# Kernel optimization log

Hardware: AMD Instinct MI355X
Metric: run time of the kernel (lower is better)

## Reference

```python
import jax, jax.numpy as jnp
import numpy as np

B, N, I = 8, 1024, 64
E, H, D = 2, 2, 128   # edge types, heads per layer, hidden dim
O = 64                # num_outputs
IN1 = E * H * D       # layer-1 filter input dim (concat of layer-0 heads)


def setup_inputs() -> dict:
    key = jax.random.key(0)
    ks = jax.random.split(key, 20)
    s = lambda f: 1.0 / np.sqrt(f)
    inp = {
        "nodes": jax.random.normal(ks[0], (B, N, I), jnp.float32),
        "edges": jax.random.normal(ks[1], (B, N, N, E), jnp.float32) * 0.1,
        "Wemb": jax.random.normal(ks[2], (I, D), jnp.float32) * s(I),
        "bemb": jnp.zeros((D,), jnp.float32),
        # layer 0 params: filter W, att nets a1/a2 (weight + bias), state bias
        "W0":   jax.random.normal(ks[3], (E, H, D, D), jnp.float32) * s(D),
        "A1w0": jax.random.normal(ks[4], (E, H, D), jnp.float32) * s(D),
        "A1b0": jnp.zeros((E, H), jnp.float32),
        "A2w0": jax.random.normal(ks[5], (E, H, D), jnp.float32) * s(D),
        "A2b0": jnp.zeros((E, H), jnp.float32),
        "SB0":  jnp.zeros((E, H, D), jnp.float32),
        # layer 1 params (input dim = E*H*D from concat)
        "W1":   jax.random.normal(ks[6], (E, H, IN1, D), jnp.float32) * s(IN1),
        "A1w1": jax.random.normal(ks[7], (E, H, D), jnp.float32) * s(D),
        "A1b1": jnp.zeros((E, H), jnp.float32),
        "A2w1": jax.random.normal(ks[8], (E, H, D), jnp.float32) * s(D),
        "A2b1": jnp.zeros((E, H), jnp.float32),
        "SB1":  jnp.zeros((E, H, D), jnp.float32),
        "Wout": jax.random.normal(ks[9], (D, O), jnp.float32) * s(D),
        "bout": jnp.zeros((O,), jnp.float32),
    }
    return inp


def _gat_layer(state, edges_ebnn, W, a1w, a1b, a2w, a2b, sb):
    # state: (B,N,Fin); W: (E,H,Fin,D); edges_ebnn: (E,1,B,N,N)
    Wh = jnp.einsum('bni,ehid->ehbnd', state, W)                    # (E,H,B,N,D)
    s1 = jnp.einsum('ehbnd,ehd->ehbn', Wh, a1w) + a1b[:, :, None, None]
    s2 = jnp.einsum('ehbnd,ehd->ehbn', Wh, a2w) + a2b[:, :, None, None]
    att = s1[..., :, None] + s2[..., None, :]                       # a1_i + a2_j
    att = jax.nn.leaky_relu(att, 0.2) + edges_ebnn                  # edge-type bias
    att = jax.nn.softmax(att, axis=-2)                              # torch dim=1 (over i)
    msg = jnp.einsum('ehbij,ehbjd->ehbid', att, Wh)                 # bmm aggregation
    return msg + sb[:, :, None, None, :]                            # (E,H,B,N,D)


def reference(nodes, edges, Wemb, bemb,
              W0, A1w0, A1b0, A2w0, A2b0, SB0,
              W1, A1w1, A1b1, A2w1, A2b1, SB1,
              Wout, bout):
    edges_e = jnp.transpose(edges, (3, 0, 1, 2))[:, None]           # (E,1,B,N,N)
    state = jax.nn.relu(nodes @ Wemb + bemb)                        # SlimFC embedding
    # layer 0: concat heads/edgetypes along feature dim (torch order jj outer, ii inner)
    m0 = _gat_layer(state, edges_e, W0, A1w0, A1b0, A2w0, A2b0, SB0)
    state = jnp.transpose(m0, (2, 3, 0, 1, 4)).reshape(B, N, E * H * D)
    # layer 1 (last): elu then mean over all heads/edgetypes
    m1 = jax.nn.elu(_gat_layer(state, edges_e, W1, A1w1, A1b1, A2w1, A2b1, SB1))
    state = jnp.mean(m1, axis=(0, 1))                               # (B,N,D)
    return state @ Wout + bout                                      # (B,N,O)
```

## Files before the change

### kernel.cpp

```cpp
#include <hip/hip_runtime.h>
#include <hip/hip_bf16.h>
#include <math.h>

#define NB 8
#define NN 1024
#define NI 64
#define EHC 4
#define ND 128
#define NO 64
#define FIN1 512
#define BN 8192

typedef __attribute__((ext_vector_type(8))) short short8;
typedef __attribute__((ext_vector_type(4))) float f32x4;

__device__ __forceinline__ unsigned short f2bf(float f) {
    union { float f; unsigned u; } v; v.f = f;
    unsigned r = v.u + 0x7FFF + ((v.u >> 16) & 1);
    return (unsigned short)(r >> 16);
}
__device__ __forceinline__ float bf2f(unsigned short h) {
    union { unsigned u; float f; } v; v.u = ((unsigned)h) << 16;
    return v.f;
}

__global__ void prepTk(const float* __restrict__ W0, const float* __restrict__ W1,
                       unsigned short* __restrict__ W0T, unsigned short* __restrict__ W1T) {
    int idx = blockIdx.x * 256 + threadIdx.x;
    if (idx < EHC * ND * ND) {
        int eh = idx >> 14, d = (idx >> 7) & 127, k = idx & 127;
        W0T[idx] = f2bf(W0[((size_t)(eh * ND + k)) * ND + d]);
    }
    int idx1 = idx - EHC * ND * ND;
    if (idx1 >= 0 && idx1 < EHC * ND * FIN1) {
        int eh = idx1 >> 16;
        int r = idx1 & 65535;
        int d = r >> 9, k = r & 511;
        W1T[idx1] = f2bf(W1[((size_t)(eh * FIN1 + k)) * ND + d]);
    }
}

__global__ __launch_bounds__(256) void embedk(const float* __restrict__ nodes,
                                              const float* __restrict__ Wemb,
                                              const float* __restrict__ bemb,
                                              unsigned short* __restrict__ state0) {
    int row0 = blockIdx.x * 16;
    int t = threadIdx.x;
    __shared__ float wL[NI * ND];
    __shared__ float nL[16 * NI];
    for (int idx = t; idx < NI * ND; idx += 256) wL[idx] = Wemb[idx];
    for (int idx = t; idx < 16 * NI; idx += 256) nL[idx] = nodes[(size_t)row0 * NI + idx];
    __syncthreads();
    int d = t & 127, rh = t >> 7;
    float b0 = bemb[d];
    float acc[8];
#pragma unroll
    for (int r = 0; r < 8; ++r) acc[r] = b0;
#pragma unroll 8
    for (int k = 0; k < NI; ++k) {
        float w = wL[k * ND + d];
#pragma unroll
        for (int r = 0; r < 8; ++r) acc[r] += nL[(rh * 8 + r) * NI + k] * w;
    }
#pragma unroll
    for (int r = 0; r < 8; ++r)
        state0[(size_t)(row0 + rh * 8 + r) * ND + d] = f2bf(fmaxf(acc[r], 0.f));
}

template <int FIN>
__global__ __launch_bounds__(256) void whgemmk(const unsigned short* __restrict__ state,
                                               const unsigned short* __restrict__ WT,
                                               unsigned short* __restrict__ WhT) {
    int eh = blockIdx.y;
    int row0 = blockIdx.x * 64;
    int t = threadIdx.x;
    int w = t >> 6, lane = t & 63;
    int m = lane & 15, quad = lane >> 4;

    f32x4 acc[4][2];
#pragma unroll
    for (int mt = 0; mt < 4; ++mt)
#pragma unroll
        for (int nt = 0; nt < 2; ++nt) acc[mt][nt] = (f32x4){0.f, 0.f, 0.f, 0.f};

    const unsigned short* Ab = state + (size_t)(row0 + m) * FIN + quad * 8;
    const unsigned short* Bb = WT + ((size_t)eh * ND + w * 32 + m) * FIN + quad * 8;
#pragma unroll
    for (int k0 = 0; k0 < FIN; k0 += 32) {
        short8 a[4], b[2];
#pragma unroll
        for (int mt = 0; mt < 4; ++mt)
            a[mt] = *(const short8*)(Ab + (size_t)mt * 16 * FIN + k0);
#pragma unroll
        for (int nt = 0; nt < 2; ++nt)
            b[nt] = *(const short8*)(Bb + (size_t)nt * 16 * FIN + k0);
#pragma unroll
        for (int mt = 0; mt < 4; ++mt)
#pragma unroll
            for (int nt = 0; nt < 2; ++nt)
                acc[mt][nt] =
                    __builtin_amdgcn_mfma_f32_16x16x32_bf16(a[mt], b[nt], acc[mt][nt], 0, 0, 0);
    }
    int b_ = row0 >> 10, i0b = row0 & 1023;
#pragma unroll
    for (int mt = 0; mt < 4; ++mt)
#pragma unroll
        for (int nt = 0; nt < 2; ++nt) {
            int d = w * 32 + nt * 16 + m;
            int i = i0b + mt * 16 + quad * 4;
            union { unsigned short us[4]; unsigned long long u64; } pk;
#pragma unroll
            for (int r = 0; r < 4; ++r) pk.us[r] = f2bf(acc[mt][nt][r]);
            *(unsigned long long*)(WhT + (((size_t)eh * NB + b_) * ND + d) * NN + i) = pk.u64;
        }
}

__global__ __launch_bounds__(256) void s1s2k(const unsigned short* __restrict__ WhT,
                                             const float* __restrict__ a1w,
                                             const float* __restrict__ a1b,
                                             const float* __restrict__ a2w,
                                             const float* __restrict__ a2b,
                                             float* __restrict__ s1, float* __restrict__ s2) {
    int bx = blockIdx.x;
    int ehb = bx >> 4;
    int eh = ehb >> 3;
    int it = bx & 15;
    int i0 = it * 64;
    int t = threadIdx.x;
    int il = t & 63, dc = t >> 6;
    const unsigned short* wp = WhT + ((size_t)ehb * ND + dc * 32) * NN + i0 + il;
    float r1 = 0.f, r2 = 0.f;
#pragma unroll 8
    for (int dd = 0; dd < 32; ++dd) {
        int d = dc * 32 + dd;
        float wv = bf2f(wp[(size_t)dd * NN]);
        r1 += wv * a1w[eh * ND + d];
        r2 += wv * a2w[eh * ND + d];
    }
    __shared__ float red[2][4][64];
    red[0][dc][il] = r1;
    red[1][dc][il] = r2;
    __syncthreads();
    if (t < 64) {
        s1[(size_t)ehb * NN + i0 + t] =
            red[0][0][t] + red[0][1][t] + red[0][2][t] + red[0][3][t] + a1b[eh];
    } else if (t < 128) {
        int il2 = t - 64;
        s2[(size_t)ehb * NN + i0 + il2] =
            red[1][0][il2] + red[1][1][il2] + red[1][2][il2] + red[1][3][il2] + a2b[eh];
    }
}

__global__ __launch_bounds__(256) void colsumk(const float* __restrict__ edges,
                                               const float* __restrict__ s1,
                                               const float* __restrict__ s2,
                                               float* __restrict__ Spart) {
    int jt = blockIdx.x, b = blockIdx.y, ic = blockIdx.z;
    int t = threadIdx.x;
    int jl = t & 63, is = t >> 6;
    int j = jt * 64 + jl;
    __shared__ float s1L[4][256];
    for (int idx = t; idx < 1024; idx += 256) {
        int eh = idx >> 8;
        s1L[eh][idx & 255] = s1[((size_t)eh * NB + b) * NN + ic * 256 + (idx & 255)];
    }
    __syncthreads();
    float s2v[4], acc4[4];
#pragma unroll
    for (int eh = 0; eh < 4; ++eh) {
        s2v[eh] = s2[((size_t)eh * NB + b) * NN + j];
        acc4[eh] = 0.f;
    }
    const float2* ep = (const float2*)edges + ((size_t)(b * NN + ic * 256 + is * 64)) * NN + j;
#pragma unroll 4
    for (int ii = 0; ii < 64; ++ii) {
        float2 ev = ep[(size_t)ii * NN];
        int il = is * 64 + ii;
#pragma unroll
        for (int eh = 0; eh < 4; ++eh) {
            float x = s1L[eh][il] + s2v[eh];
            x = x >= 0.f ? x : 0.2f * x;
            float a = x + (eh < 2 ? ev.x : ev.y);
            acc4[eh] += __expf(a);
        }
    }
    __shared__ float red[4][4][64];
#pragma unroll
    for (int eh = 0; eh < 4; ++eh) red[is][eh][jl] = acc4[eh];
    __syncthreads();
    if (t < 256) {
        int eho = t >> 6, jlo = t & 63;
        float Sv = red[0][eho][jlo] + red[1][eho][jlo] + red[2][eho][jlo] + red[3][eho][jlo];
        Spart[(((size_t)ic * EHC + eho) * NB + b) * NN + jt * 64 + jlo] = Sv;
    }
}

__global__ __launch_bounds__(256, 2) void msgk(const float* __restrict__ edges,
                                               const unsigned short* __restrict__ WhT,
                                               const float* __restrict__ s1,
                                               const float* __restrict__ s2,
                                               const float* __restrict__ Spart,
                                               const float* __restrict__ sb,
                                               unsigned short* __restrict__ out0,
                                               float* __restrict__ out1, int mode) {
    int eh = blockIdx.x, itile = blockIdx.y, b = blockIdx.z;
    int e = eh >> 1;
    int i0 = itile * 64;
    int t = threadIdx.x;
    int w = t >> 6, lane = t & 63;
    int n = lane & 15, quad = lane >> 4;
    int jl = t & 63, ib = w;

    __shared__ float2 stL[NN];
    __shared__ unsigned short pA[2][64 * 72];

    int base = (eh * NB + b) * NN;
    for (int idx = t; idx < NN; idx += 256) {
        float Sv = Spart[((size_t)(0 * EHC + eh) * NB + b) * NN + idx] +
                   Spart[((size_t)(1 * EHC + eh) * NB + b) * NN + idx] +
                   Spart[((size_t)(2 * EHC + eh) * NB + b) * NN + idx] +
                   Spart[((size_t)(3 * EHC + eh) * NB + b) * NN + idx];
        stL[idx] = make_float2(s2[base + idx], 1.f / Sv);
    }
    float s1r[16];
    {
        const f32x4* sp = (const f32x4*)(s1 + base + i0 + ib * 16);
#pragma unroll
        for (int q4 = 0; q4 < 4; ++q4) {
            f32x4 v = sp[q4];
#pragma unroll
            for (int r = 0; r < 4; ++r) s1r[q4 * 4 + r] = v[r];
        }
    }

    f32x4 acc[2][4];
#pragma unroll
    for (int mt = 0; mt < 2; ++mt)
#pragma unroll
        for (int nt = 0; nt < 4; ++nt) acc[mt][nt] = (f32x4){0.f, 0.f, 0.f, 0.f};

    const unsigned short* Ab =
        WhT + ((size_t)(eh * NB + b) * ND + (w * 32 + n)) * NN + quad * 8;
    const float2* ep = (const float2*)edges + (size_t)(b * NN + i0 + ib * 16) * NN + jl;
    __syncthreads();

    float2 evA[16], evB[16];
    short8 aA[4], aB[4];

    auto loadE = [&](float2* ev, int j0) {
#pragma unroll
        for (int q = 0; q < 16; ++q) ev[q] = ep[(size_t)q * NN + j0];
    };
    auto loadA = [&](short8* av, int j0) {
#pragma unroll
        for (int mt = 0; mt < 2; ++mt)
#pragma unroll
            for (int kt = 0; kt < 2; ++kt)
                av[mt * 2 + kt] = *(const short8*)(Ab + (size_t)mt * 16 * NN + kt * 32 + j0);
    };
    auto pstep = [&](const float2* ev, const short8* av, int j0, int buf) {
        float2 st = stL[j0 + jl];
#pragma unroll
        for (int q = 0; q < 16; ++q) {
            float edge = e ? ev[q].y : ev[q].x;
            float x = s1r[q] + st.x;
            x = x >= 0.f ? x : 0.2f * x;
            pA[buf][(ib * 16 + q) * 72 + jl] = f2bf(__expf(x + edge) * st.y);
        }
        __syncthreads();
        short8 bv[4][2];
#pragma unroll
        for (int nt = 0; nt < 4; ++nt)
#pragma unroll
            for (int kt = 0; kt < 2; ++kt)
                bv[nt][kt] = *(const short8*)&pA[buf][(nt * 16 + n) * 72 + kt * 32 + quad * 8];
#pragma unroll
        for (int kt = 0; kt < 2; ++kt)
#pragma unroll
            for (int mt = 0; mt < 2; ++mt)
#pragma unroll
                for (int nt = 0; nt < 4; ++nt)
                    acc[mt][nt] = __builtin_amdgcn_mfma_f32_16x16x32_bf16(
                        av[mt * 2 + kt], bv[nt][kt], acc[mt][nt], 0, 0, 0);
    };

    loadE(evA, 0);
    loadA(aA, 0);
    for (int sp2 = 0; sp2 < 8; ++sp2) {
        int j0 = sp2 * 128;
        loadE(evB, j0 + 64);
        loadA(aB, j0 + 64);
        pstep(evA, aA, j0, 0);
        if (sp2 < 7) {
            loadE(evA, j0 + 128);
            loadA(aA, j0 + 128);
        }
        pstep(evB, aB, j0 + 64, 1);
    }

#pragma unroll
    for (int mt = 0; mt < 2; ++mt) {
        int d0 = w * 32 + mt * 16 + quad * 4;
        f32x4 sbv = *(const f32x4*)&sb[eh * ND + d0];
#pragma unroll
        for (int nt = 0; nt < 4; ++nt) {
            int i = i0 + nt * 16 + n;
            if (mode == 0) {
                union { unsigned short us[4]; unsigned long long u64; } pk;
#pragma unroll
                for (int r = 0; r < 4; ++r) pk.us[r] = f2bf(acc[mt][nt][r] + sbv[r]);
                *(unsigned long long*)(out0 + (size_t)(b * NN + i) * FIN1 + eh * ND + d0) =
                    pk.u64;
            } else {
                f32x4 vv;
#pragma unroll
                for (int r = 0; r < 4; ++r) {
                    float v = acc[mt][nt][r] + sbv[r];
                    vv[r] = v > 0.f ? v : expm1f(v);
                }
                *(f32x4*)(out1 + ((size_t)(eh * NB + b) * NN + i) * ND + d0) = vv;
            }
        }
    }
}

__global__ __launch_bounds__(256) void finalk(const float* __restrict__ m1,
                                              const float* __restrict__ Wout,
                                              const float* __restrict__ bout,
                                              float* __restrict__ out) {
    int row0 = blockIdx.x * 16;
    int t = threadIdx.x;
    __shared__ float sF[16 * ND];
    __shared__ float wL[ND * NO];
    const size_t str = (size_t)BN * ND;
    for (int idx = t; idx < 16 * ND; idx += 256) {
        size_t r = (size_t)row0 * ND + idx;
        sF[idx] = 0.25f * (m1[r] + m1[r + str] + m1[r + 2 * str] + m1[r + 3 * str]);
    }
    for (int idx = t; idx < ND * NO; idx += 256) wL[idx] = Wout[idx];
    __syncthreads();
    int o = t & 63;
    int rr = t >> 6;
    float bo = bout[o];
#pragma unroll
    for (int q = 0; q < 4; ++q) {
        int r = rr * 4 + q;
        float acc = 0.f;
#pragma unroll 4
        for (int d = 0; d < ND; ++d) acc += sF[r * ND + d] * wL[d * NO + o];
        out[(size_t)(row0 + r) * NO + o] = acc + bo;
    }
}

extern "C" void kernel_launch(void* const* d_in, const int* in_sizes, int n_in,
                              void* d_out, int out_size, void* d_ws, size_t ws_size,
                              hipStream_t stream) {
    const float* nodes = (const float*)d_in[0];
    const float* edges = (const float*)d_in[1];
    const float* Wemb = (const float*)d_in[2];
    const float* bemb = (const float*)d_in[3];
    const float* W0 = (const float*)d_in[4];
    const float* A1w0 = (const float*)d_in[5];
    const float* A1b0 = (const float*)d_in[6];
    const float* A2w0 = (const float*)d_in[7];
    const float* A2b0 = (const float*)d_in[8];
    const float* SB0 = (const float*)d_in[9];
    const float* W1 = (const float*)d_in[10];
    const float* A1w1 = (const float*)d_in[11];
    const float* A1b1 = (const float*)d_in[12];
    const float* A2w1 = (const float*)d_in[13];
    const float* A2b1 = (const float*)d_in[14];
    const float* SB1 = (const float*)d_in[15];
    const float* Wout = (const float*)d_in[16];
    const float* bout = (const float*)d_in[17];
    float* out = (float*)d_out;

    char* p = (char*)d_ws;
    auto alloc = [&](size_t bytes) {
        char* r = p;
        p += (bytes + 255) & ~(size_t)255;
        return r;
    };
    unsigned short* state0 = (unsigned short*)alloc((size_t)BN * ND * 2);
    unsigned short* W0T = (unsigned short*)alloc((size_t)EHC * ND * ND * 2);
    unsigned short* W1T = (unsigned short*)alloc((size_t)EHC * ND * FIN1 * 2);
    unsigned short* WhT = (unsigned short*)alloc((size_t)EHC * BN * ND * 2);
    unsigned short* state1 = (unsigned short*)alloc((size_t)BN * FIN1 * 2);
    float* s1b = (float*)alloc((size_t)EHC * BN * 4);
    float* s2b = (float*)alloc((size_t)EHC * BN * 4);
    float* Spart = (float*)alloc((size_t)4 * EHC * BN * 4);
    float* m1 = (float*)alloc((size_t)EHC * BN * ND * 4);

    prepTk<<<1280, 256, 0, stream>>>(W0, W1, W0T, W1T);
    embedk<<<BN / 16, 256, 0, stream>>>(nodes, Wemb, bemb, state0);
    whgemmk<ND><<<dim3(BN / 64, EHC), 256, 0, stream>>>(state0, W0T, WhT);
    s1s2k<<<512, 256, 0, stream>>>(WhT, A1w0, A1b0, A2w0, A2b0, s1b, s2b);
    colsumk<<<dim3(NN / 64, NB, 4), 256, 0, stream>>>(edges, s1b, s2b, Spart);
    msgk<<<dim3(EHC, NN / 64, NB), 256, 0, stream>>>(edges, WhT, s1b, s2b, Spart, SB0,
                                                     state1, m1, 0);
    whgemmk<FIN1><<<dim3(BN / 64, EHC), 256, 0, stream>>>(state1, W1T, WhT);
    s1s2k<<<512, 256, 0, stream>>>(WhT, A1w1, A1b1, A2w1, A2b1, s1b, s2b);
    colsumk<<<dim3(NN / 64, NB, 4), 256, 0, stream>>>(edges, s1b, s2b, Spart);
    msgk<<<dim3(EHC, NN / 64, NB), 256, 0, stream>>>(edges, WhT, s1b, s2b, Spart, SB1,
                                                     state1, m1, 1);
    finalk<<<BN / 16, 256, 0, stream>>>(m1, Wout, bout, out);
}
```

Baseline: 309.2 us.

## Fuse attention scores into Wh GEMM, shrink tiles, precompute log column sums

The s1/s2 attention-score dot products move into the Wh GEMM epilogue, using wave shuffles and a shared reduction, which removes a separate kernel and its re-read of WhT. Row tiles in the GEMM, column-sum and message kernels are halved and occupancy hints raised to spread work across more blocks. A small new kernel sums eight column-sum partials and stores log(S), so the message kernel folds normalization into the exponent instead of multiplying by a reciprocal. Smaller message tiles mean WhT and edges are re-read more often per output row, and one extra kernel launch is added.

```diff
diff --git a/kernel.cpp b/kernel.cpp
--- a/kernel.cpp
+++ b/kernel.cpp
@@ -68,18 +68,24 @@
 }
 
 template <int FIN>
-__global__ __launch_bounds__(256) void whgemmk(const unsigned short* __restrict__ state,
-                                               const unsigned short* __restrict__ WT,
-                                               unsigned short* __restrict__ WhT) {
+__global__ __launch_bounds__(256, 4) void whgemmk(const unsigned short* __restrict__ state,
+                                                  const unsigned short* __restrict__ WT,
+                                                  unsigned short* __restrict__ WhT,
+                                                  const float* __restrict__ a1w,
+                                                  const float* __restrict__ a1b,
+                                                  const float* __restrict__ a2w,
+                                                  const float* __restrict__ a2b,
+                                                  float* __restrict__ s1,
+                                                  float* __restrict__ s2) {
     int eh = blockIdx.y;
-    int row0 = blockIdx.x * 64;
+    int row0 = blockIdx.x * 32;
     int t = threadIdx.x;
     int w = t >> 6, lane = t & 63;
     int m = lane & 15, quad = lane >> 4;
 
-    f32x4 acc[4][2];
-#pragma unroll
-    for (int mt = 0; mt < 4; ++mt)
+    f32x4 acc[2][2];
+#pragma unroll
+    for (int mt = 0; mt < 2; ++mt)
 #pragma unroll
         for (int nt = 0; nt < 2; ++nt) acc[mt][nt] = (f32x4){0.f, 0.f, 0.f, 0.f};
 
@@ -87,23 +93,24 @@
     const unsigned short* Bb = WT + ((size_t)eh * ND + w * 32 + m) * FIN + quad * 8;
 #pragma unroll
     for (int k0 = 0; k0 < FIN; k0 += 32) {
-        short8 a[4], b[2];
-#pragma unroll
-        for (int mt = 0; mt < 4; ++mt)
+        short8 a[2], b[2];
+#pragma unroll
+        for (int mt = 0; mt < 2; ++mt)
             a[mt] = *(const short8*)(Ab + (size_t)mt * 16 * FIN + k0);
 #pragma unroll
         for (int nt = 0; nt < 2; ++nt)
             b[nt] = *(const short8*)(Bb + (size_t)nt * 16 * FIN + k0);
 #pragma unroll
-        for (int mt = 0; mt < 4; ++mt)
+        for (int mt = 0; mt < 2; ++mt)
 #pragma unroll
             for (int nt = 0; nt < 2; ++nt)
                 acc[mt][nt] =
                     __builtin_amdgcn_mfma_f32_16x16x32_bf16(a[mt], b[nt], acc[mt][nt], 0, 0, 0);
     }
     int b_ = row0 >> 10, i0b = row0 & 1023;
-#pragma unroll
-    for (int mt = 0; mt < 4; ++mt)
+    int ehb = eh * NB + b_;
+#pragma unroll
+    for (int mt = 0; mt < 2; ++mt)
 #pragma unroll
         for (int nt = 0; nt < 2; ++nt) {
             int d = w * 32 + nt * 16 + m;
@@ -111,58 +118,66 @@
             union { unsigned short us[4]; unsigned long long u64; } pk;
 #pragma unroll
             for (int r = 0; r < 4; ++r) pk.us[r] = f2bf(acc[mt][nt][r]);
-            *(unsigned long long*)(WhT + (((size_t)eh * NB + b_) * ND + d) * NN + i) = pk.u64;
-        }
-}
-
-__global__ __launch_bounds__(256) void s1s2k(const unsigned short* __restrict__ WhT,
-                                             const float* __restrict__ a1w,
-                                             const float* __restrict__ a1b,
-                                             const float* __restrict__ a2w,
-                                             const float* __restrict__ a2b,
-                                             float* __restrict__ s1, float* __restrict__ s2) {
-    int bx = blockIdx.x;
-    int ehb = bx >> 4;
-    int eh = ehb >> 3;
-    int it = bx & 15;
-    int i0 = it * 64;
-    int t = threadIdx.x;
-    int il = t & 63, dc = t >> 6;
-    const unsigned short* wp = WhT + ((size_t)ehb * ND + dc * 32) * NN + i0 + il;
-    float r1 = 0.f, r2 = 0.f;
-#pragma unroll 8
-    for (int dd = 0; dd < 32; ++dd) {
-        int d = dc * 32 + dd;
-        float wv = bf2f(wp[(size_t)dd * NN]);
-        r1 += wv * a1w[eh * ND + d];
-        r2 += wv * a2w[eh * ND + d];
-    }
-    __shared__ float red[2][4][64];
-    red[0][dc][il] = r1;
-    red[1][dc][il] = r2;
-    __syncthreads();
-    if (t < 64) {
-        s1[(size_t)ehb * NN + i0 + t] =
-            red[0][0][t] + red[0][1][t] + red[0][2][t] + red[0][3][t] + a1b[eh];
-    } else if (t < 128) {
-        int il2 = t - 64;
-        s2[(size_t)ehb * NN + i0 + il2] =
-            red[1][0][il2] + red[1][1][il2] + red[1][2][il2] + red[1][3][il2] + a2b[eh];
-    }
-}
-
-__global__ __launch_bounds__(256) void colsumk(const float* __restrict__ edges,
-                                               const float* __restrict__ s1,
-                                               const float* __restrict__ s2,
-                                               float* __restrict__ Spart) {
+            *(unsigned long long*)(WhT + (((size_t)ehb) * ND + d) * NN + i) = pk.u64;
+        }
+    float w1a = a1w[eh * ND + w * 32 + m], w1b = a1w[eh * ND + w * 32 + 16 + m];
+    float w2a = a2w[eh * ND + w * 32 + m], w2b = a2w[eh * ND + w * 32 + 16 + m];
+    float p1[2][4], p2[2][4];
+#pragma unroll
+    for (int mt = 0; mt < 2; ++mt)
+#pragma unroll
+        for (int r = 0; r < 4; ++r) {
+            p1[mt][r] = acc[mt][0][r] * w1a + acc[mt][1][r] * w1b;
+            p2[mt][r] = acc[mt][0][r] * w2a + acc[mt][1][r] * w2b;
+        }
+#pragma unroll
+    for (int off = 8; off >= 1; off >>= 1)
+#pragma unroll
+        for (int mt = 0; mt < 2; ++mt)
+#pragma unroll
+            for (int r = 0; r < 4; ++r) {
+                p1[mt][r] += __shfl_xor(p1[mt][r], off);
+                p2[mt][r] += __shfl_xor(p2[mt][r], off);
+            }
+    __shared__ float sred[2][4][4][8];
+    if (m == 0) {
+#pragma unroll
+        for (int mt = 0; mt < 2; ++mt)
+#pragma unroll
+            for (int r = 0; r < 4; ++r) {
+                sred[0][w][quad][mt * 4 + r] = p1[mt][r];
+                sred[1][w][quad][mt * 4 + r] = p2[mt][r];
+            }
+    }
+    __syncthreads();
+    if (t < 32) {
+        int mt = t >> 4, quad2 = (t >> 2) & 3, r = t & 3;
+        int c = mt * 4 + r;
+        float v = sred[0][0][quad2][c] + sred[0][1][quad2][c] + sred[0][2][quad2][c] +
+                  sred[0][3][quad2][c];
+        s1[(size_t)ehb * NN + i0b + t] = v + a1b[eh];
+    } else if (t < 64) {
+        int tl = t - 32;
+        int mt = tl >> 4, quad2 = (tl >> 2) & 3, r = tl & 3;
+        int c = mt * 4 + r;
+        float v = sred[1][0][quad2][c] + sred[1][1][quad2][c] + sred[1][2][quad2][c] +
+                  sred[1][3][quad2][c];
+        s2[(size_t)ehb * NN + i0b + tl] = v + a2b[eh];
+    }
+}
+
+__global__ __launch_bounds__(256, 4) void colsumk(const float* __restrict__ edges,
+                                                  const float* __restrict__ s1,
+                                                  const float* __restrict__ s2,
+                                                  float* __restrict__ Spart) {
     int jt = blockIdx.x, b = blockIdx.y, ic = blockIdx.z;
     int t = threadIdx.x;
     int jl = t & 63, is = t >> 6;
     int j = jt * 64 + jl;
-    __shared__ float s1L[4][256];
-    for (int idx = t; idx < 1024; idx += 256) {
-        int eh = idx >> 8;
-        s1L[eh][idx & 255] = s1[((size_t)eh * NB + b) * NN + ic * 256 + (idx & 255)];
+    __shared__ float s1L[4][128];
+    for (int idx = t; idx < 512; idx += 256) {
+        int eh = idx >> 7;
+        s1L[eh][idx & 127] = s1[((size_t)eh * NB + b) * NN + ic * 128 + (idx & 127)];
     }
     __syncthreads();
     float s2v[4], acc4[4];
@@ -171,11 +186,11 @@
         s2v[eh] = s2[((size_t)eh * NB + b) * NN + j];
         acc4[eh] = 0.f;
     }
-    const float2* ep = (const float2*)edges + ((size_t)(b * NN + ic * 256 + is * 64)) * NN + j;
+    const float2* ep = (const float2*)edges + ((size_t)(b * NN + ic * 128 + is * 32)) * NN + j;
 #pragma unroll 4
-    for (int ii = 0; ii < 64; ++ii) {
+    for (int ii = 0; ii < 32; ++ii) {
         float2 ev = ep[(size_t)ii * NN];
-        int il = is * 64 + ii;
+        int il = is * 32 + ii;
 #pragma unroll
         for (int eh = 0; eh < 4; ++eh) {
             float x = s1L[eh][il] + s2v[eh];
@@ -195,61 +210,62 @@
     }
 }
 
-__global__ __launch_bounds__(256, 2) void msgk(const float* __restrict__ edges,
+__global__ __launch_bounds__(256) void s2adjk(const float* __restrict__ Spart,
+                                              float* __restrict__ lnS) {
+    int gid = blockIdx.x * 256 + threadIdx.x;
+    const size_t str = (size_t)EHC * NB * NN;
+    float S = 0.f;
+#pragma unroll
+    for (int ic = 0; ic < 8; ++ic) S += Spart[(size_t)ic * str + gid];
+    lnS[gid] = __logf(S);
+}
+
+__global__ __launch_bounds__(256, 4) void msgk(const float* __restrict__ edges,
                                                const unsigned short* __restrict__ WhT,
                                                const float* __restrict__ s1,
                                                const float* __restrict__ s2,
-                                               const float* __restrict__ Spart,
+                                               const float* __restrict__ lnS,
                                                const float* __restrict__ sb,
                                                unsigned short* __restrict__ out0,
                                                float* __restrict__ out1, int mode) {
     int eh = blockIdx.x, itile = blockIdx.y, b = blockIdx.z;
     int e = eh >> 1;
-    int i0 = itile * 64;
+    int i0 = itile * 32;
     int t = threadIdx.x;
     int w = t >> 6, lane = t & 63;
     int n = lane & 15, quad = lane >> 4;
-    int jl = t & 63, ib = w;
+    int jl = t & 63, ib = t >> 6;
 
     __shared__ float2 stL[NN];
-    __shared__ unsigned short pA[2][64 * 72];
+    __shared__ unsigned short pA[2][32 * 72];
 
     int base = (eh * NB + b) * NN;
-    for (int idx = t; idx < NN; idx += 256) {
-        float Sv = Spart[((size_t)(0 * EHC + eh) * NB + b) * NN + idx] +
-                   Spart[((size_t)(1 * EHC + eh) * NB + b) * NN + idx] +
-                   Spart[((size_t)(2 * EHC + eh) * NB + b) * NN + idx] +
-                   Spart[((size_t)(3 * EHC + eh) * NB + b) * NN + idx];
-        stL[idx] = make_float2(s2[base + idx], 1.f / Sv);
-    }
-    float s1r[16];
+    for (int idx = t; idx < NN; idx += 256)
+        stL[idx] = make_float2(s2[base + idx], lnS[base + idx]);
+    float s1r[8];
     {
-        const f32x4* sp = (const f32x4*)(s1 + base + i0 + ib * 16);
-#pragma unroll
-        for (int q4 = 0; q4 < 4; ++q4) {
-            f32x4 v = sp[q4];
-#pragma unroll
-            for (int r = 0; r < 4; ++r) s1r[q4 * 4 + r] = v[r];
-        }
-    }
-
-    f32x4 acc[2][4];
+        const f32x4* sp = (const f32x4*)(s1 + base + i0 + ib * 8);
+        f32x4 v0 = sp[0], v1 = sp[1];
+#pragma unroll
+        for (int r = 0; r < 4; ++r) { s1r[r] = v0[r]; s1r[r + 4] = v1[r]; }
+    }
+
+    f32x4 acc[2][2];
 #pragma unroll
     for (int mt = 0; mt < 2; ++mt)
 #pragma unroll
-        for (int nt = 0; nt < 4; ++nt) acc[mt][nt] = (f32x4){0.f, 0.f, 0.f, 0.f};
-
-    const unsigned short* Ab =
-        WhT + ((size_t)(eh * NB + b) * ND + (w * 32 + n)) * NN + quad * 8;
-    const float2* ep = (const float2*)edges + (size_t)(b * NN + i0 + ib * 16) * NN + jl;
-    __syncthreads();
-
-    float2 evA[16], evB[16];
+        for (int nt = 0; nt < 2; ++nt) acc[mt][nt] = (f32x4){0.f, 0.f, 0.f, 0.f};
+
+    const unsigned short* Ab = WhT + ((size_t)base * ND + (size_t)(w * 32 + n) * NN) + quad * 8;
+    const float2* ep = (const float2*)edges + (size_t)(b * NN + i0 + ib * 8) * NN + jl;
+    __syncthreads();
+
+    float2 evA[8], evB[8];
     short8 aA[4], aB[4];
 
     auto loadE = [&](float2* ev, int j0) {
 #pragma unroll
-        for (int q = 0; q < 16; ++q) ev[q] = ep[(size_t)q * NN + j0];
+        for (int q = 0; q < 8; ++q) ev[q] = ep[(size_t)q * NN + j0];
     };
     auto loadA = [&](short8* av, int j0) {
 #pragma unroll
@@ -261,16 +277,16 @@
     auto pstep = [&](const float2* ev, const short8* av, int j0, int buf) {
         float2 st = stL[j0 + jl];
 #pragma unroll
-        for (int q = 0; q < 16; ++q) {
+        for (int q = 0; q < 8; ++q) {
             float edge = e ? ev[q].y : ev[q].x;
             float x = s1r[q] + st.x;
             x = x >= 0.f ? x : 0.2f * x;
-            pA[buf][(ib * 16 + q) * 72 + jl] = f2bf(__expf(x + edge) * st.y);
+            pA[buf][(ib * 8 + q) * 72 + jl] = f2bf(__expf(x + edge - st.y));
         }
         __syncthreads();
-        short8 bv[4][2];
-#pragma unroll
-        for (int nt = 0; nt < 4; ++nt)
+        short8 bv[2][2];
+#pragma unroll
+        for (int nt = 0; nt < 2; ++nt)
 #pragma unroll
             for (int kt = 0; kt < 2; ++kt)
                 bv[nt][kt] = *(const short8*)&pA[buf][(nt * 16 + n) * 72 + kt * 32 + quad * 8];
@@ -279,7 +295,7 @@
 #pragma unroll
             for (int mt = 0; mt < 2; ++mt)
 #pragma unroll
-                for (int nt = 0; nt < 4; ++nt)
+                for (int nt = 0; nt < 2; ++nt)
                     acc[mt][nt] = __builtin_amdgcn_mfma_f32_16x16x32_bf16(
                         av[mt * 2 + kt], bv[nt][kt], acc[mt][nt], 0, 0, 0);
     };
@@ -303,7 +319,7 @@
         int d0 = w * 32 + mt * 16 + quad * 4;
         f32x4 sbv = *(const f32x4*)&sb[eh * ND + d0];
 #pragma unroll
-        for (int nt = 0; nt < 4; ++nt) {
+        for (int nt = 0; nt < 2; ++nt) {
             int i = i0 + nt * 16 + n;
             if (mode == 0) {
                 union { unsigned short us[4]; unsigned long long u64; } pk;
@@ -388,20 +404,23 @@
     unsigned short* state1 = (unsigned short*)alloc((size_t)BN * FIN1 * 2);
     float* s1b = (float*)alloc((size_t)EHC * BN * 4);
     float* s2b = (float*)alloc((size_t)EHC * BN * 4);
-    float* Spart = (float*)alloc((size_t)4 * EHC * BN * 4);
+    float* Spart = (float*)alloc((size_t)8 * EHC * BN * 4);
+    float* lnSb = (float*)alloc((size_t)EHC * BN * 4);
     float* m1 = (float*)alloc((size_t)EHC * BN * ND * 4);
 
     prepTk<<<1280, 256, 0, stream>>>(W0, W1, W0T, W1T);
     embedk<<<BN / 16, 256, 0, stream>>>(nodes, Wemb, bemb, state0);
-    whgemmk<ND><<<dim3(BN / 64, EHC), 256, 0, stream>>>(state0, W0T, WhT);
-    s1s2k<<<512, 256, 0, stream>>>(WhT, A1w0, A1b0, A2w0, A2b0, s1b, s2b);
-    colsumk<<<dim3(NN / 64, NB, 4), 256, 0, stream>>>(edges, s1b, s2b, Spart);
-    msgk<<<dim3(EHC, NN / 64, NB), 256, 0, stream>>>(edges, WhT, s1b, s2b, Spart, SB0,
+    whgemmk<ND><<<dim3(BN / 32, EHC), 256, 0, stream>>>(state0, W0T, WhT, A1w0, A1b0, A2w0,
+                                                        A2b0, s1b, s2b);
+    colsumk<<<dim3(NN / 64, NB, 8), 256, 0, stream>>>(edges, s1b, s2b, Spart);
+    s2adjk<<<EHC * BN / 256, 256, 0, stream>>>(Spart, lnSb);
+    msgk<<<dim3(EHC, NN / 32, NB), 256, 0, stream>>>(edges, WhT, s1b, s2b, lnSb, SB0,
                                                      state1, m1, 0);
-    whgemmk<FIN1><<<dim3(BN / 64, EHC), 256, 0, stream>>>(state1, W1T, WhT);
-    s1s2k<<<512, 256, 0, stream>>>(WhT, A1w1, A1b1, A2w1, A2b1, s1b, s2b);
-    colsumk<<<dim3(NN / 64, NB, 4), 256, 0, stream>>>(edges, s1b, s2b, Spart);
-    msgk<<<dim3(EHC, NN / 64, NB), 256, 0, stream>>>(edges, WhT, s1b, s2b, Spart, SB1,
+    whgemmk<FIN1><<<dim3(BN / 32, EHC), 256, 0, stream>>>(state1, W1T, WhT, A1w1, A1b1, A2w1,
+                                                          A2b1, s1b, s2b);
+    colsumk<<<dim3(NN / 64, NB, 8), 256, 0, stream>>>(edges, s1b, s2b, Spart);
+    s2adjk<<<EHC * BN / 256, 256, 0, stream>>>(Spart, lnSb);
+    msgk<<<dim3(EHC, NN / 32, NB), 256, 0, stream>>>(edges, WhT, s1b, s2b, lnSb, SB1,
                                                      state1, m1, 1);
     finalk<<<BN / 16, 256, 0, stream>>>(m1, Wout, bout, out);
 }
```

Measured after the change: 329.4 us. 1.07x slower.
